# Kernel tuning notes

Hardware: AMD Instinct MI355X
Metric: run time of the kernel (lower is better)

## Reference

```python
import jax, jax.numpy as jnp
import numpy as np

B, N, E = 8, 2048, 1024


def setup_inputs() -> dict:
    key = jax.random.key(0)
    x = jax.random.normal(key, (B, N, E), dtype=jnp.float32)
    pos = jnp.ones((N - 1,), dtype=jnp.float32)
    zero = jnp.ones((1,), dtype=jnp.float32)
    neg = jnp.ones((N - 1,), dtype=jnp.float32)
    return {"x": x, "pos": pos, "zero": zero, "neg": neg}


def reference(x, pos, zero, neg):
    # x: [b, n, e]; Toeplitz matvec via circular FFT convolution of length 2n.
    b, n, e = x.shape
    # circulant kernel: [zero, pos[:n-1], zero, neg[-(n-1):]] -> length 2n
    a = jnp.concatenate([zero, pos[: n - 1], zero, neg[-(n - 1):]])
    # torch: fft(x, 2n, dim=1, norm='ortho')
    y = jnp.fft.fft(x, n=2 * n, axis=1, norm="ortho")  # [b, 2n, e] complex
    # torch: fft(a) with default ('backward') norm, i.e. unnormalized forward
    v = jnp.fft.fft(a)[None, :, None]                   # [1, 2n, 1]
    u = v * y
    out = jnp.fft.ifft(u, n=2 * n, axis=1, norm="ortho")[:, :n, :].real
    return out.astype(x.dtype)
```

## Files before the change

### kernel.cpp

```cpp
#include <hip/hip_runtime.h>
#include <stdint.h>


#define B_  8
#define N_  2048
#define E_  1024

typedef __bf16 bf16x8 __attribute__((ext_vector_type(8)));
typedef float  f32x4  __attribute__((ext_vector_type(4)));

__device__ __forceinline__ unsigned short f32_to_bf16_rne(float f) {
    union { float f; unsigned int u; } cv; cv.f = f;
    unsigned int u = cv.u;
    u += 0x7fffu + ((u >> 16) & 1u);
    return (unsigned short)(u >> 16);
}

__global__ __launch_bounds__(256) void build_T(const float* __restrict__ pos,
                                               const float* __restrict__ zero,
                                               const float* __restrict__ neg,
                                               unsigned short* __restrict__ T) {
    int t  = blockIdx.x * 256 + threadIdx.x;
    int k  = t >> 8;
    int j0 = (t & 255) * 8;
    float zv = zero[0];
    union { unsigned short s[8]; uint4 v; } pk;
#pragma unroll
    for (int i = 0; i < 8; ++i) {
        int j = j0 + i;
        float v = (j < k) ? pos[k - j - 1]
                : (j == k) ? zv
                : neg[N_ - 1 - j + k];
        pk.s[i] = f32_to_bf16_rne(v);
    }
    *(uint4*)(T + (size_t)k * N_ + j0) = pk.v;
}

__global__ __launch_bounds__(256) void transpose_x(const float* __restrict__ x,
                                                   unsigned short* __restrict__ xT) {
    __shared__ float tile[64][66];
    int b  = blockIdx.z;
    int j0 = blockIdx.y * 64;
    int e0 = blockIdx.x * 64;
    int t  = threadIdx.x;

    int e4 = t & 15, jr = t >> 4;
#pragma unroll
    for (int it = 0; it < 4; ++it) {
        int j = jr + it * 16;
        const float4 v = *(const float4*)(x + ((size_t)(b * N_ + j0 + j) * E_) + e0 + e4 * 4);
        tile[e4 * 4 + 0][j] = v.x;
        tile[e4 * 4 + 1][j] = v.y;
        tile[e4 * 4 + 2][j] = v.z;
        tile[e4 * 4 + 3][j] = v.w;
    }
    __syncthreads();
    int j2 = (t & 31) * 2, er = t >> 5;
#pragma unroll
    for (int it = 0; it < 8; ++it) {
        int e = er + it * 8;
        float2 v = *(const float2*)&tile[e][j2];
        union { unsigned short s[2]; unsigned int u; } pk;
        pk.s[0] = f32_to_bf16_rne(v.x);
        pk.s[1] = f32_to_bf16_rne(v.y);
        *(unsigned int*)(xT + ((size_t)(b * E_ + e0 + e)) * N_ + j0 + j2) = pk.u;
    }
}

#define BK  64
#define LDT 72

__global__ __launch_bounds__(256) void gemm_toep(const unsigned short* __restrict__ T,
                                                 const unsigned short* __restrict__ xT,
                                                 float* __restrict__ out) {
    __shared__ __align__(16) unsigned short As[128 * LDT];
    __shared__ __align__(16) unsigned short Bs[128 * LDT];

    int bid = blockIdx.x;
    int b   = bid >> 7;
    int mt  = (bid >> 3) & 15;
    int nt  = bid & 7;
    int m0  = mt * 128, n0 = nt * 128;

    int t    = threadIdx.x;
    int lane = t & 63;
    int w    = t >> 6;
    int wr   = w >> 1, wc = w & 1;
    int lm   = lane & 15, quad = lane >> 4;

    const unsigned short* Ag = T + (size_t)m0 * N_;
    const unsigned short* Bg = xT + (size_t)(b * E_ + n0) * N_;

    int srow = t >> 3;
    int scol = (t & 7) * 8;

    f32x4 acc[4][4] = {};

    for (int kt = 0; kt < N_ / BK; ++kt) {
        int kbase = kt * BK;
        __syncthreads();
#pragma unroll
        for (int it = 0; it < 4; ++it) {
            int r = srow + it * 32;
            uint4 av = *(const uint4*)(Ag + (size_t)r * N_ + kbase + scol);
            uint4 bv = *(const uint4*)(Bg + (size_t)r * N_ + kbase + scol);
            *(uint4*)(As + r * LDT + scol) = av;
            *(uint4*)(Bs + r * LDT + scol) = bv;
        }
        __syncthreads();
#pragma unroll
        for (int kh = 0; kh < 2; ++kh) {
            int ko = kh * 32;
            bf16x8 af[4], bfr[4];
#pragma unroll
            for (int i = 0; i < 4; ++i) {
                af[i]  = *(const bf16x8*)(As + (wr * 64 + i * 16 + lm) * LDT + ko + quad * 8);
                bfr[i] = *(const bf16x8*)(Bs + (wc * 64 + i * 16 + lm) * LDT + ko + quad * 8);
            }
#pragma unroll
            for (int i = 0; i < 4; ++i)
#pragma unroll
                for (int jn = 0; jn < 4; ++jn)
                    acc[i][jn] = __builtin_amdgcn_mfma_f32_16x16x32_bf16(af[i], bfr[jn], acc[i][jn], 0, 0, 0);
        }
    }

    float* Og = out + ((size_t)(b * N_ + m0)) * E_ + n0;
#pragma unroll
    for (int i = 0; i < 4; ++i) {
#pragma unroll
        for (int jn = 0; jn < 4; ++jn) {
            int e = wc * 64 + jn * 16 + lm;
#pragma unroll
            for (int r = 0; r < 4; ++r) {
                int k = wr * 64 + i * 16 + quad * 4 + r;
                Og[(size_t)k * E_ + e] = acc[i][jn][r];
            }
        }
    }
}

__global__ __launch_bounds__(256) void naive_toep(const float* __restrict__ x,
                                                  const float* __restrict__ pos,
                                                  const float* __restrict__ zero,
                                                  const float* __restrict__ neg,
                                                  float* __restrict__ out) {
    int bid = blockIdx.x;
    int e   = (bid & 3) * 256 + threadIdx.x;
    int k   = (bid >> 2) & (N_ - 1);
    int b   = bid >> 13;
    float zv = zero[0];
    float acc = 0.f;
    const float* xb = x + (size_t)b * N_ * E_ + e;
    for (int j = 0; j < N_; ++j) {
        float c = (j < k) ? pos[k - j - 1] : (j == k) ? zv : neg[N_ - 1 - j + k];
        acc += c * xb[(size_t)j * E_];
    }
    out[((size_t)(b * N_ + k)) * E_ + e] = acc;
}

extern "C" void kernel_launch(void* const* d_in, const int* in_sizes, int n_in,
                              void* d_out, int out_size, void* d_ws, size_t ws_size,
                              hipStream_t stream) {
    const float* x    = (const float*)d_in[0];
    const float* pos  = (const float*)d_in[1];
    const float* zero = (const float*)d_in[2];
    const float* neg  = (const float*)d_in[3];
    float* out = (float*)d_out;

    const size_t needT = (size_t)N_ * N_ * sizeof(unsigned short);
    const size_t needX = (size_t)B_ * E_ * N_ * sizeof(unsigned short);
    if (ws_size >= needT + needX) {
        unsigned short* T  = (unsigned short*)d_ws;
        unsigned short* xT = (unsigned short*)d_ws + (size_t)N_ * N_;
        build_T<<<2048, 256, 0, stream>>>(pos, zero, neg, T);
        transpose_x<<<dim3(16, 32, 8), 256, 0, stream>>>(x, xT);
        gemm_toep<<<1024, 256, 0, stream>>>(T, xT, out);
    } else {
        naive_toep<<<65536, 256, 0, stream>>>(x, pos, zero, neg, out);
    }
}
```

Baseline: 205.4 us.

## Replace dense Toeplitz GEMM with shared-memory radix-16 FFT convolution

Result: no change. 201.8 us (-1.7%).

```diff
diff --git a/kernel.cpp b/kernel.cpp
--- a/kernel.cpp
+++ b/kernel.cpp
@@ -2,12 +2,14 @@
 #include <stdint.h>
 
 
-#define B_  8
-#define N_  2048
-#define E_  1024
-
-typedef __bf16 bf16x8 __attribute__((ext_vector_type(8)));
-typedef float  f32x4  __attribute__((ext_vector_type(4)));
+#define B_ 8
+#define N_ 2048
+#define NF 4096
+#define E_ 1024
+
+#define BUFSZ (NF + (NF >> 5))
+__device__ __forceinline__ int P(int n) { return n + (n >> 5); }
+#define PERM(r) ((((r) & 3) << 2) | ((r) >> 2))
 
 __device__ __forceinline__ unsigned short f32_to_bf16_rne(float f) {
     union { float f; unsigned int u; } cv; cv.f = f;
@@ -15,25 +17,127 @@
     u += 0x7fffu + ((u >> 16) & 1u);
     return (unsigned short)(u >> 16);
 }
-
-__global__ __launch_bounds__(256) void build_T(const float* __restrict__ pos,
+__device__ __forceinline__ float bf16_to_f32(unsigned short u) {
+    union { unsigned int u; float f; } cv; cv.u = ((unsigned int)u) << 16; return cv.f;
+}
+__device__ __forceinline__ void cmul(float& ar, float& ai, float br, float bi) {
+    float t = ar * br - ai * bi; ai = ar * bi + ai * br; ar = t;
+}
+
+__device__ __forceinline__ void dft4(float& x0r, float& x0i, float& x1r, float& x1i,
+                                     float& x2r, float& x2i, float& x3r, float& x3i,
+                                     float sg) {
+    float t0r = x0r + x2r, t0i = x0i + x2i;
+    float t1r = x0r - x2r, t1i = x0i - x2i;
+    float t2r = x1r + x3r, t2i = x1i + x3i;
+    float t3r = x1r - x3r, t3i = x1i - x3i;
+    x0r = t0r + t2r; x0i = t0i + t2i;
+    x2r = t0r - t2r; x2i = t0i - t2i;
+    x1r = t1r - sg * t3i; x1i = t1i + sg * t3r;
+    x3r = t1r + sg * t3i; x3i = t1i - sg * t3r;
+}
+
+template<int SG>
+__device__ __forceinline__ void dft16(float* xr, float* xi) {
+    const float sg = (float)SG;
+#pragma unroll
+    for (int n0 = 0; n0 < 4; ++n0)
+        dft4(xr[n0], xi[n0], xr[n0 + 4], xi[n0 + 4],
+             xr[n0 + 8], xi[n0 + 8], xr[n0 + 12], xi[n0 + 12], sg);
+    const float C1 = 0.923879532511286756f;
+    const float S1 = 0.382683432365089772f;
+    const float H  = 0.707106781186547524f;
+    cmul(xr[5],  xi[5],  C1,  sg * S1);
+    cmul(xr[9],  xi[9],  H,   sg * H);
+    cmul(xr[13], xi[13], S1,  sg * C1);
+    cmul(xr[6],  xi[6],  H,   sg * H);
+    cmul(xr[10], xi[10], 0.f, sg);
+    cmul(xr[14], xi[14], -H,  sg * H);
+    cmul(xr[7],  xi[7],  S1,  sg * C1);
+    cmul(xr[11], xi[11], -H,  sg * H);
+    cmul(xr[15], xi[15], -C1, -sg * S1);
+#pragma unroll
+    for (int k1 = 0; k1 < 4; ++k1)
+        dft4(xr[4 * k1], xi[4 * k1], xr[4 * k1 + 1], xi[4 * k1 + 1],
+             xr[4 * k1 + 2], xi[4 * k1 + 2], xr[4 * k1 + 3], xi[4 * k1 + 3], sg);
+}
+
+template<int INV, int L>
+__device__ __forceinline__ void fft_stage(float2* buf, const float2* __restrict__ tw2, int t) {
+    constexpr int Lq = L / 16;
+    int g = t / Lq;
+    int j = t - g * Lq;
+    int base = g * L + j;
+    float xr[16], xi[16];
+#pragma unroll
+    for (int r = 0; r < 16; ++r) {
+        float2 v = buf[P(base + r * Lq)];
+        xr[r] = v.x; xi[r] = v.y;
+    }
+    float2 w1 = tw2[j * (NF / L)];
+    float w1r = w1.x, w1i = INV ? -w1.y : w1.y;
+    if (INV) {
+        float wr = 1.f, wi = 0.f;
+#pragma unroll
+        for (int r = 1; r < 16; ++r) { cmul(wr, wi, w1r, w1i); cmul(xr[r], xi[r], wr, wi); }
+        dft16<1>(xr, xi);
+#pragma unroll
+        for (int r = 0; r < 16; ++r) {
+            float2 v; v.x = xr[PERM(r)]; v.y = xi[PERM(r)];
+            buf[P(base + r * Lq)] = v;
+        }
+    } else {
+        dft16<-1>(xr, xi);
+        { float2 v; v.x = xr[0]; v.y = xi[0]; buf[P(base)] = v; }
+        float wr = 1.f, wi = 0.f;
+#pragma unroll
+        for (int r = 1; r < 16; ++r) {
+            cmul(wr, wi, w1r, w1i);
+            float yr = xr[PERM(r)], yi = xi[PERM(r)];
+            cmul(yr, yi, wr, wi);
+            float2 v; v.x = yr; v.y = yi;
+            buf[P(base + r * Lq)] = v;
+        }
+    }
+}
+
+__global__ __launch_bounds__(256) void build_tw(float2* tw2) {
+    int k = blockIdx.x * 256 + threadIdx.x;
+    double th = -6.283185307179586476925286766559 * (double)k / 4096.0;
+    float2 v; v.x = (float)cos(th); v.y = (float)sin(th);
+    tw2[k] = v;
+}
+
+__global__ __launch_bounds__(256) void build_V(const float* __restrict__ pos,
                                                const float* __restrict__ zero,
                                                const float* __restrict__ neg,
-                                               unsigned short* __restrict__ T) {
-    int t  = blockIdx.x * 256 + threadIdx.x;
-    int k  = t >> 8;
-    int j0 = (t & 255) * 8;
-    float zv = zero[0];
-    union { unsigned short s[8]; uint4 v; } pk;
-#pragma unroll
-    for (int i = 0; i < 8; ++i) {
-        int j = j0 + i;
-        float v = (j < k) ? pos[k - j - 1]
-                : (j == k) ? zv
-                : neg[N_ - 1 - j + k];
-        pk.s[i] = f32_to_bf16_rne(v);
-    }
-    *(uint4*)(T + (size_t)k * N_ + j0) = pk.v;
+                                               const float2* __restrict__ tw2,
+                                               float2* __restrict__ V2) {
+    __shared__ float2 buf[BUFSZ];
+    int t = threadIdx.x;
+#pragma unroll
+    for (int it = 0; it < 16; ++it) {
+        int n = t + 256 * it;
+        float v;
+        if (n == 0) v = zero[0];
+        else if (n < N_) v = pos[n - 1];
+        else if (n == N_) v = zero[0];
+        else v = neg[n - (N_ + 1)];
+        float2 c; c.x = v; c.y = 0.f;
+        buf[P(n)] = c;
+    }
+    __syncthreads();
+    fft_stage<0, 4096>(buf, tw2, t); __syncthreads();
+    fft_stage<0, 256>(buf, tw2, t);  __syncthreads();
+    fft_stage<0, 16>(buf, tw2, t);   __syncthreads();
+    const float s = 1.f / (float)NF;
+#pragma unroll
+    for (int it = 0; it < 16; ++it) {
+        int n = t + 256 * it;
+        float2 c = buf[P(n)];
+        c.x *= s; c.y *= s;
+        V2[n] = c;
+    }
 }
 
 __global__ __launch_bounds__(256) void transpose_x(const float* __restrict__ x,
@@ -67,76 +171,77 @@
     }
 }
 
-#define BK  64
-#define LDT 72
-
-__global__ __launch_bounds__(256) void gemm_toep(const unsigned short* __restrict__ T,
-                                                 const unsigned short* __restrict__ xT,
-                                                 float* __restrict__ out) {
-    __shared__ __align__(16) unsigned short As[128 * LDT];
-    __shared__ __align__(16) unsigned short Bs[128 * LDT];
-
+__global__ __launch_bounds__(256) void fft_conv(const unsigned short* __restrict__ xT,
+                                                const float2* __restrict__ tw2,
+                                                const float2* __restrict__ V2,
+                                                float* __restrict__ out) {
+    __shared__ float2 buf[BUFSZ];
+    int t = threadIdx.x;
     int bid = blockIdx.x;
-    int b   = bid >> 7;
-    int mt  = (bid >> 3) & 15;
-    int nt  = bid & 7;
-    int m0  = mt * 128, n0 = nt * 128;
-
-    int t    = threadIdx.x;
-    int lane = t & 63;
-    int w    = t >> 6;
-    int wr   = w >> 1, wc = w & 1;
-    int lm   = lane & 15, quad = lane >> 4;
-
-    const unsigned short* Ag = T + (size_t)m0 * N_;
-    const unsigned short* Bg = xT + (size_t)(b * E_ + n0) * N_;
-
-    int srow = t >> 3;
-    int scol = (t & 7) * 8;
-
-    f32x4 acc[4][4] = {};
-
-    for (int kt = 0; kt < N_ / BK; ++kt) {
-        int kbase = kt * BK;
-        __syncthreads();
-#pragma unroll
-        for (int it = 0; it < 4; ++it) {
-            int r = srow + it * 32;
-            uint4 av = *(const uint4*)(Ag + (size_t)r * N_ + kbase + scol);
-            uint4 bv = *(const uint4*)(Bg + (size_t)r * N_ + kbase + scol);
-            *(uint4*)(As + r * LDT + scol) = av;
-            *(uint4*)(Bs + r * LDT + scol) = bv;
-        }
-        __syncthreads();
-#pragma unroll
-        for (int kh = 0; kh < 2; ++kh) {
-            int ko = kh * 32;
-            bf16x8 af[4], bfr[4];
-#pragma unroll
-            for (int i = 0; i < 4; ++i) {
-                af[i]  = *(const bf16x8*)(As + (wr * 64 + i * 16 + lm) * LDT + ko + quad * 8);
-                bfr[i] = *(const bf16x8*)(Bs + (wc * 64 + i * 16 + lm) * LDT + ko + quad * 8);
-            }
-#pragma unroll
-            for (int i = 0; i < 4; ++i)
-#pragma unroll
-                for (int jn = 0; jn < 4; ++jn)
-                    acc[i][jn] = __builtin_amdgcn_mfma_f32_16x16x32_bf16(af[i], bfr[jn], acc[i][jn], 0, 0, 0);
-        }
-    }
-
-    float* Og = out + ((size_t)(b * N_ + m0)) * E_ + n0;
+    int xcd = bid & 7;
+    int q = bid >> 3;
+    int b = q >> 6;
+    int ep = xcd * 64 + (q & 63);
+    int e0 = ep * 2;
+
+    const unsigned short* r0 = xT + ((size_t)(b * E_ + e0)) * N_;
+    uint4 u0 = ((const uint4*)r0)[t];
+    uint4 u1 = ((const uint4*)(r0 + N_))[t];
+    unsigned int a0[4] = { u0.x, u0.y, u0.z, u0.w };
+    unsigned int a1[4] = { u1.x, u1.y, u1.z, u1.w };
 #pragma unroll
     for (int i = 0; i < 4; ++i) {
-#pragma unroll
-        for (int jn = 0; jn < 4; ++jn) {
-            int e = wc * 64 + jn * 16 + lm;
-#pragma unroll
-            for (int r = 0; r < 4; ++r) {
-                int k = wr * 64 + i * 16 + quad * 4 + r;
-                Og[(size_t)k * E_ + e] = acc[i][jn][r];
-            }
-        }
+        int n = 8 * t + 2 * i;
+        float2 c0; c0.x = bf16_to_f32((unsigned short)(a0[i] & 0xffff));
+        c0.y = bf16_to_f32((unsigned short)(a1[i] & 0xffff));
+        buf[P(n)] = c0;
+        float2 c1; c1.x = bf16_to_f32((unsigned short)(a0[i] >> 16));
+        c1.y = bf16_to_f32((unsigned short)(a1[i] >> 16));
+        buf[P(n + 1)] = c1;
+    }
+#pragma unroll
+    for (int it = 0; it < 8; ++it) {
+        int n = N_ + t + 256 * it;
+        float2 z; z.x = 0.f; z.y = 0.f;
+        buf[P(n)] = z;
+    }
+    __syncthreads();
+    fft_stage<0, 4096>(buf, tw2, t); __syncthreads();
+    fft_stage<0, 256>(buf, tw2, t);  __syncthreads();
+    {
+        int base = 16 * t;
+        float xr[16], xi[16];
+#pragma unroll
+        for (int r = 0; r < 16; ++r) {
+            float2 v = buf[P(base + r)];
+            xr[r] = v.x; xi[r] = v.y;
+        }
+        dft16<-1>(xr, xi);
+        float yr[16], yi[16];
+#pragma unroll
+        for (int r = 0; r < 16; ++r) {
+            float2 vv = V2[base + r];
+            float ar = xr[PERM(r)], ai = xi[PERM(r)];
+            yr[r] = ar * vv.x - ai * vv.y;
+            yi[r] = ar * vv.y + ai * vv.x;
+        }
+        dft16<1>(yr, yi);
+#pragma unroll
+        for (int r = 0; r < 16; ++r) {
+            float2 v; v.x = yr[PERM(r)]; v.y = yi[PERM(r)];
+            buf[P(base + r)] = v;
+        }
+    }
+    __syncthreads();
+    fft_stage<1, 256>(buf, tw2, t);  __syncthreads();
+    fft_stage<1, 4096>(buf, tw2, t); __syncthreads();
+
+    float* ob = out + ((size_t)b * N_) * E_ + e0;
+#pragma unroll
+    for (int it = 0; it < 8; ++it) {
+        int k = t + 256 * it;
+        float2 v = buf[P(k)];
+        *(float2*)(ob + (size_t)k * E_) = v;
     }
 }
 
@@ -168,14 +273,16 @@
     const float* neg  = (const float*)d_in[3];
     float* out = (float*)d_out;
 
-    const size_t needT = (size_t)N_ * N_ * sizeof(unsigned short);
     const size_t needX = (size_t)B_ * E_ * N_ * sizeof(unsigned short);
-    if (ws_size >= needT + needX) {
-        unsigned short* T  = (unsigned short*)d_ws;
-        unsigned short* xT = (unsigned short*)d_ws + (size_t)N_ * N_;
-        build_T<<<2048, 256, 0, stream>>>(pos, zero, neg, T);
+    const size_t need  = needX + 2 * (size_t)NF * sizeof(float2);
+    if (ws_size >= need) {
+        unsigned short* xT = (unsigned short*)d_ws;
+        float2* tw2 = (float2*)((char*)d_ws + needX);
+        float2* V2  = tw2 + NF;
+        build_tw<<<16, 256, 0, stream>>>(tw2);
         transpose_x<<<dim3(16, 32, 8), 256, 0, stream>>>(x, xT);
-        gemm_toep<<<1024, 256, 0, stream>>>(T, xT, out);
+        build_V<<<1, 256, 0, stream>>>(pos, zero, neg, tw2, V2);
+        fft_conv<<<4096, 256, 0, stream>>>(xT, tw2, V2, out);
     } else {
         naive_toep<<<65536, 256, 0, stream>>>(x, pos, zero, neg, out);
     }
```
